# Kernel optimization log

Measured on AMD Instinct MI355X. Metric: run time of the kernel, lower is better.

## Reference

```python
import jax, jax.numpy as jnp
import numpy as np

B, S, HID = 2, 2048, 2048
NH = 16
Q_LORA, KV_LORA = 1024, 512
NOPE, ROPE, VD = 128, 64, 128
QK = NOPE + ROPE  # 192
EPS = 1e-6
THETA = 10000.0


def rms_norm(x, w, eps=EPS):
    x32 = x.astype(jnp.float32)
    var = jnp.mean(x32 * x32, axis=-1, keepdims=True)
    return (w * (x32 * jax.lax.rsqrt(var + eps))).astype(x.dtype)


def rotate_half(x):
    h = x.shape[-1] // 2
    return jnp.concatenate([-x[..., h:], x[..., :h]], axis=-1)


def setup_inputs() -> dict:
    key = jax.random.key(0)
    ks = jax.random.split(key, 8)
    hidden_states = jax.random.normal(ks[0], (B, S, HID), dtype=jnp.float32)
    attention_mask = jnp.zeros((B, 1, 1, S), dtype=jnp.float32)
    # RoPE tables (true rotary values)
    inv_freq = 1.0 / (THETA ** (np.arange(0, ROPE, 2, dtype=np.float32) / ROPE))
    pos = np.arange(S, dtype=np.float32)
    freqs = np.outer(pos, inv_freq)  # [S, ROPE/2]
    emb = np.concatenate([freqs, freqs], axis=-1)  # [S, ROPE]
    cos = jnp.asarray(np.cos(emb), dtype=jnp.float32)
    sin = jnp.asarray(np.sin(emb), dtype=jnp.float32)
    # Parameters, stored as [in, out] so y = x @ W
    sd = lambda fan_in: 1.0 / np.sqrt(fan_in)
    w_q_down = jax.random.normal(ks[1], (HID, Q_LORA), dtype=jnp.float32) * sd(HID)
    w_q_up = jax.random.normal(ks[2], (Q_LORA, NH * QK), dtype=jnp.float32) * sd(Q_LORA)
    w_kv_down = jax.random.normal(ks[3], (HID, KV_LORA + ROPE), dtype=jnp.float32) * sd(HID)
    w_kv_up = jax.random.normal(ks[4], (KV_LORA, NH * (NOPE + VD)), dtype=jnp.float32) * sd(KV_LORA)
    w_o = jax.random.normal(ks[5], (NH * VD, HID), dtype=jnp.float32) * sd(NH * VD)
    q_norm_w = jnp.ones((Q_LORA,), dtype=jnp.float32)
    kv_norm_w = jnp.ones((KV_LORA,), dtype=jnp.float32)
    return dict(hidden_states=hidden_states, attention_mask=attention_mask,
                cos=cos, sin=sin, w_q_down=w_q_down, w_q_up=w_q_up,
                w_kv_down=w_kv_down, w_kv_up=w_kv_up, w_o=w_o,
                q_norm_w=q_norm_w, kv_norm_w=kv_norm_w)


def reference(hidden_states, attention_mask, cos, sin,
              w_q_down, w_q_up, w_kv_down, w_kv_up, w_o,
              q_norm_w, kv_norm_w):
    b, s, _ = hidden_states.shape
    # --- Q path: down-proj -> RMSNorm -> up-proj ---
    q = rms_norm(hidden_states @ w_q_down, q_norm_w) @ w_q_up  # [b,s,NH*QK]
    q = q.reshape(b, s, NH, QK).transpose(0, 2, 1, 3)          # [b,h,s,QK]
    q_nope, q_rope = q[..., :NOPE], q[..., NOPE:]
    # --- KV path: down-proj -> split latent / rope key -> up-proj ---
    kv = hidden_states @ w_kv_down                              # [b,s,KV_LORA+ROPE]
    kv_latent, k_rope = kv[..., :KV_LORA], kv[..., KV_LORA:]
    kv_up = rms_norm(kv_latent, kv_norm_w) @ w_kv_up            # [b,s,NH*(NOPE+VD)]
    kv_up = kv_up.reshape(b, s, NH, NOPE + VD).transpose(0, 2, 1, 3)
    k_nope, v = kv_up[..., :NOPE], kv_up[..., NOPE:]            # [b,h,s,*]
    k_rope = k_rope[:, None, :, :]                              # [b,1,s,ROPE] (broadcast over heads)
    # --- partial RoPE ---
    c = cos[None, None, :, :]
    sn = sin[None, None, :, :]
    q_rope = q_rope * c + rotate_half(q_rope) * sn
    k_rope = k_rope * c + rotate_half(k_rope) * sn
    q_final = jnp.concatenate([q_nope, q_rope], axis=-1)        # [b,h,s,QK]
    k_final = jnp.concatenate([k_nope, jnp.broadcast_to(k_rope, (b, NH, s, ROPE))], axis=-1)
    # --- SDPA (non-causal, additive mask) ---
    scale = 1.0 / jnp.sqrt(jnp.asarray(QK, dtype=jnp.float32))
    scores = jnp.einsum('bhqd,bhkd->bhqk', q_final, k_final) * scale
    scores = scores + attention_mask                            # [b,1,1,s] broadcast
    probs = jax.nn.softmax(scores.astype(jnp.float32), axis=-1).astype(q_final.dtype)
    attn = jnp.einsum('bhqk,bhkd->bhqd', probs, v)              # [b,h,s,VD]
    attn = attn.transpose(0, 2, 1, 3).reshape(b, s, NH * VD)
    return attn @ w_o
```

## Files before the change

### kernel.cpp

```cpp
#include <hip/hip_runtime.h>
#include <hip/hip_bf16.h>

typedef unsigned short u16;
typedef unsigned int u32;
typedef short s16x8 __attribute__((ext_vector_type(8)));
typedef float f32x4 __attribute__((ext_vector_type(4)));
typedef float f32x2 __attribute__((ext_vector_type(2)));

__device__ __forceinline__ float bf2f(u16 u) {
    union { u32 i; float f; } v; v.i = ((u32)u) << 16; return v.f;
}
__device__ __forceinline__ u16 f2bf(float f) {
    union { float f; u32 i; } v; v.f = f;
    u32 i = v.i;
    u32 r = (i + 0x7FFFu + ((i >> 16) & 1u)) >> 16;
    return (u16)r;
}

__device__ __forceinline__ void gl2lds16(const u16* g, u16* l) {
    __builtin_amdgcn_global_load_lds(
        (const __attribute__((address_space(1))) u32*)g,
        (__attribute__((address_space(3))) u32*)l, 16, 0, 0);
}

__global__ __launch_bounds__(256) void cvt_f32_bf16(
    const float* __restrict__ in, u16* __restrict__ out, long long n2)
{
    long long i = (long long)blockIdx.x * 256 + threadIdx.x;
    if (i < n2) {
        f32x2 v = *(const f32x2*)(in + i * 2);
        u32 p = (u32)f2bf(v[0]) | ((u32)f2bf(v[1]) << 16);
        *(u32*)(out + i * 2) = p;
    }
}

__global__ __launch_bounds__(256) void transpose_f32_bf16(
    const float* __restrict__ in, u16* __restrict__ out, int R, int C)
{
    __shared__ u16 t[32][33];
    int tx = threadIdx.x & 31, ty = threadIdx.x >> 5;
    int c0 = blockIdx.x * 32, r0 = blockIdx.y * 32;
    #pragma unroll
    for (int i = 0; i < 32; i += 8)
        t[ty + i][tx] = f2bf(in[(size_t)(r0 + ty + i) * C + c0 + tx]);
    __syncthreads();
    #pragma unroll
    for (int i = 0; i < 32; i += 8)
        out[(size_t)(c0 + ty + i) * R + r0 + tx] = t[tx][ty + i];
}

__global__ __launch_bounds__(256) void transpose_v(
    const u16* __restrict__ kvup, u16* __restrict__ vt)
{
    __shared__ u16 t[32][33];
    int tx = threadIdx.x & 31, ty = threadIdx.x >> 5;
    int s0 = blockIdx.x * 32, v0 = blockIdx.y * 32;
    int b = blockIdx.z >> 4, h = blockIdx.z & 15;
    #pragma unroll
    for (int i = 0; i < 32; i += 8)
        t[ty + i][tx] = kvup[(size_t)(b * 2048 + s0 + ty + i) * 4096 + h * 256 + 128 + v0 + tx];
    __syncthreads();
    #pragma unroll
    for (int i = 0; i < 32; i += 8)
        vt[((size_t)(b * 16 + h) * 128 + v0 + ty + i) * 2048 + s0 + tx] = t[tx][ty + i];
}

__global__ __launch_bounds__(256) void gemm_bf16(
    const u16* __restrict__ A, const u16* __restrict__ Bt, u16* __restrict__ C,
    int M, int N, int K)
{
    __shared__ u16 As[64][40];
    __shared__ u16 Bs[64][40];

    const int tid  = threadIdx.x;
    const int wave = tid >> 6, lane = tid & 63;
    const int quad = lane >> 4, l16 = lane & 15;
    const int m0 = blockIdx.y * 64, n0 = blockIdx.x * 64;
    const int wm = (wave >> 1) * 32, wn = (wave & 1) * 32;

    const int srow = tid >> 2;
    const int koff = (tid & 3) * 8;

    f32x4 acc00 = {0.f,0.f,0.f,0.f};
    f32x4 acc01 = {0.f,0.f,0.f,0.f};
    f32x4 acc10 = {0.f,0.f,0.f,0.f};
    f32x4 acc11 = {0.f,0.f,0.f,0.f};

    for (int k0 = 0; k0 < K; k0 += 32) {
        *(s16x8*)&As[srow][koff] = *(const s16x8*)&A[(size_t)(m0 + srow) * K + k0 + koff];
        *(s16x8*)&Bs[srow][koff] = *(const s16x8*)&Bt[(size_t)(n0 + srow) * K + k0 + koff];
        __syncthreads();
        s16x8 a0 = *(const s16x8*)&As[wm + l16][quad * 8];
        s16x8 a1 = *(const s16x8*)&As[wm + 16 + l16][quad * 8];
        s16x8 b0 = *(const s16x8*)&Bs[wn + l16][quad * 8];
        s16x8 b1 = *(const s16x8*)&Bs[wn + 16 + l16][quad * 8];
        acc00 = __builtin_amdgcn_mfma_f32_16x16x32_bf16(a0, b0, acc00, 0, 0, 0);
        acc01 = __builtin_amdgcn_mfma_f32_16x16x32_bf16(a0, b1, acc01, 0, 0, 0);
        acc10 = __builtin_amdgcn_mfma_f32_16x16x32_bf16(a1, b0, acc10, 0, 0, 0);
        acc11 = __builtin_amdgcn_mfma_f32_16x16x32_bf16(a1, b1, acc11, 0, 0, 0);
        __syncthreads();
    }

    #pragma unroll
    for (int r = 0; r < 4; ++r) {
        int row0 = m0 + wm + quad * 4 + r;
        int col0 = n0 + wn + l16;
        C[(size_t)row0 * N + col0]             = f2bf(acc00[r]);
        C[(size_t)row0 * N + col0 + 16]        = f2bf(acc01[r]);
        C[(size_t)(row0 + 16) * N + col0]      = f2bf(acc10[r]);
        C[(size_t)(row0 + 16) * N + col0 + 16] = f2bf(acc11[r]);
    }
}

template <typename OUT>
__global__ __launch_bounds__(256) void gemm128(
    const u16* __restrict__ A, const u16* __restrict__ Bt, OUT* __restrict__ C,
    int M, int N, int K)
{
    __shared__ u16 As[128 * 32];
    __shared__ u16 Bs[128 * 32];

    const int tid  = threadIdx.x;
    const int wave = tid >> 6, lane = tid & 63;
    const int quad = lane >> 4, l16 = lane & 15;
    const int m0 = blockIdx.y * 128, n0 = blockIdx.x * 128;
    const int wm = (wave >> 1) * 64, wn = (wave & 1) * 64;

    const int srow = lane >> 2, soct = (lane & 3) * 8;

    f32x4 acc[4][4];
    #pragma unroll
    for (int i = 0; i < 4; ++i)
        #pragma unroll
        for (int j = 0; j < 4; ++j) acc[i][j] = (f32x4){0.f,0.f,0.f,0.f};

    for (int k0 = 0; k0 < K; k0 += 32) {
        #pragma unroll
        for (int op = 0; op < 2; ++op) {
            int g = wave * 2 + op;
            gl2lds16(&A[(size_t)(m0 + g * 16 + srow) * K + k0 + soct], &As[g * 512]);
            gl2lds16(&Bt[(size_t)(n0 + g * 16 + srow) * K + k0 + soct], &Bs[g * 512]);
        }
        __syncthreads();
        s16x8 af[4], bf[4];
        #pragma unroll
        for (int i = 0; i < 4; ++i) {
            af[i] = *(const s16x8*)&As[(wm + i * 16 + l16) * 32 + quad * 8];
            bf[i] = *(const s16x8*)&Bs[(wn + i * 16 + l16) * 32 + quad * 8];
        }
        #pragma unroll
        for (int i = 0; i < 4; ++i)
            #pragma unroll
            for (int j = 0; j < 4; ++j)
                acc[i][j] = __builtin_amdgcn_mfma_f32_16x16x32_bf16(af[i], bf[j], acc[i][j], 0, 0, 0);
        __syncthreads();
    }

    #pragma unroll
    for (int i = 0; i < 4; ++i) {
        #pragma unroll
        for (int j = 0; j < 4; ++j) {
            #pragma unroll
            for (int r = 0; r < 4; ++r) {
                int row = m0 + wm + i * 16 + quad * 4 + r;
                int col = n0 + wn + j * 16 + l16;
                if constexpr (sizeof(OUT) == 2)
                    C[(size_t)row * N + col] = f2bf(acc[i][j][r]);
                else
                    C[(size_t)row * N + col] = acc[i][j][r];
            }
        }
    }
}

__global__ __launch_bounds__(256) void rmsnorm_kernel(
    const u16* __restrict__ in, const float* __restrict__ w, u16* __restrict__ out,
    int len, int istride, int ostride)
{
    const int row = blockIdx.x, tid = threadIdx.x;
    const u16* x = in + (size_t)row * istride;
    float ss = 0.f;
    for (int i = tid; i < len; i += 256) { float v = bf2f(x[i]); ss += v * v; }
    #pragma unroll
    for (int off = 32; off >= 1; off >>= 1) ss += __shfl_xor(ss, off, 64);
    __shared__ float wsum[4];
    if ((tid & 63) == 0) wsum[tid >> 6] = ss;
    __syncthreads();
    float tot = wsum[0] + wsum[1] + wsum[2] + wsum[3];
    float inv = 1.0f / sqrtf(tot / (float)len + 1e-6f);
    for (int i = tid; i < len; i += 256) {
        float v = bf2f(x[i]);
        out[(size_t)row * ostride + i] = f2bf(v * inv * w[i]);
    }
}

__global__ __launch_bounds__(256) void rope_kernel(
    u16* __restrict__ qb, const u16* __restrict__ kvb, u16* __restrict__ krot,
    const float* __restrict__ cosb, const float* __restrict__ sinb)
{
    const int row = blockIdx.x;
    const int s = row & 2047;
    const int lane = threadIdx.x & 63, wave = threadIdx.x >> 6;
    const float c  = cosb[s * 64 + lane];
    const float sn = sinb[s * 64 + lane];
    for (int seg = wave; seg < 17; seg += 4) {
        const u16* pin; u16* pout;
        if (seg < 16) { pout = qb + (size_t)row * 3072 + seg * 192 + 128; pin = pout; }
        else          { pin = kvb + (size_t)row * 576 + 512; pout = krot + (size_t)row * 64; }
        float x  = bf2f(pin[lane]);
        float xp = bf2f(pin[lane ^ 32]);
        float rot = (lane < 32) ? -xp : xp;
        pout[lane] = f2bf(x * c + rot * sn);
    }
}

__global__ __launch_bounds__(256) void attn_mfma2(
    const u16* __restrict__ qb,
    const u16* __restrict__ kvup,
    const u16* __restrict__ krot,
    const u16* __restrict__ vt,
    const float* __restrict__ mask,
    u16* __restrict__ attnb)
{
    __shared__ u16 Ks[64][200];
    __shared__ u16 Vs[128][72];
    __shared__ u16 Ps[64][72];

    const int tid  = threadIdx.x;
    const int wave = tid >> 6, lane = tid & 63;
    const int quad = lane >> 4, l16 = lane & 15;
    const int qt = blockIdx.x, h = blockIdx.y, b = blockIdx.z;
    const int row0 = b * 2048 + qt * 64;
    const int qw = wave * 16;
    const float scale = 0.07216878364870323f;

    s16x8 qf[6];
    #pragma unroll
    for (int kc = 0; kc < 6; ++kc)
        qf[kc] = *(const s16x8*)&qb[(size_t)(row0 + qw + l16) * 3072 + h * 192 + kc * 32 + quad * 8];

    float m[4], l[4];
    #pragma unroll
    for (int r = 0; r < 4; ++r) { m[r] = -__builtin_inff(); l[r] = 0.f; }
    f32x4 O[8];
    #pragma unroll
    for (int vi = 0; vi < 8; ++vi) O[vi] = (f32x4){0.f,0.f,0.f,0.f};

    const u16* vtb = vt + ((size_t)(b * 16 + h) * 128) * 2048;

    for (int kt = 0; kt < 32; ++kt) {
        const int krow0 = b * 2048 + kt * 64;
        __syncthreads();
        #pragma unroll
        for (int i = 0; i < 6; ++i) {
            int idx = tid + i * 256;
            int r = idx / 24, c = (idx % 24) * 8;
            const u16* src = (c < 128)
                ? &kvup[(size_t)(krow0 + r) * 4096 + h * 256 + c]
                : &krot[(size_t)(krow0 + r) * 64 + (c - 128)];
            *(s16x8*)&Ks[r][c] = *(const s16x8*)src;
        }
        #pragma unroll
        for (int i = 0; i < 4; ++i) {
            int idx = tid + i * 256;
            int r = idx >> 3, c8 = (idx & 7) * 8;
            *(s16x8*)&Vs[r][c8] = *(const s16x8*)&vtb[(size_t)r * 2048 + kt * 64 + c8];
        }
        __syncthreads();

        f32x4 S[4];
        #pragma unroll
        for (int ct = 0; ct < 4; ++ct) S[ct] = (f32x4){0.f,0.f,0.f,0.f};
        #pragma unroll
        for (int kc = 0; kc < 6; ++kc) {
            #pragma unroll
            for (int ct = 0; ct < 4; ++ct) {
                s16x8 bf = *(const s16x8*)&Ks[ct * 16 + l16][kc * 32 + quad * 8];
                S[ct] = __builtin_amdgcn_mfma_f32_16x16x32_bf16(qf[kc], bf, S[ct], 0, 0, 0);
            }
        }
        #pragma unroll
        for (int ct = 0; ct < 4; ++ct) {
            float mv = mask[b * 2048 + kt * 64 + ct * 16 + l16];
            #pragma unroll
            for (int r = 0; r < 4; ++r) S[ct][r] = S[ct][r] * scale + mv;
        }
        float tmax[4];
        #pragma unroll
        for (int r = 0; r < 4; ++r)
            tmax[r] = fmaxf(fmaxf(S[0][r], S[1][r]), fmaxf(S[2][r], S[3][r]));
        #pragma unroll
        for (int off = 1; off < 16; off <<= 1) {
            #pragma unroll
            for (int r = 0; r < 4; ++r)
                tmax[r] = fmaxf(tmax[r], __shfl_xor(tmax[r], off, 64));
        }
        float alpha[4];
        #pragma unroll
        for (int r = 0; r < 4; ++r) {
            float mn = fmaxf(m[r], tmax[r]);
            alpha[r] = __expf(m[r] - mn);
            m[r] = mn;
        }
        float rsum[4] = {0.f, 0.f, 0.f, 0.f};
        #pragma unroll
        for (int ct = 0; ct < 4; ++ct) {
            #pragma unroll
            for (int r = 0; r < 4; ++r) {
                float p = __expf(S[ct][r] - m[r]);
                S[ct][r] = p;
                rsum[r] += p;
            }
        }
        #pragma unroll
        for (int off = 1; off < 16; off <<= 1) {
            #pragma unroll
            for (int r = 0; r < 4; ++r)
                rsum[r] += __shfl_xor(rsum[r], off, 64);
        }
        #pragma unroll
        for (int r = 0; r < 4; ++r) l[r] = l[r] * alpha[r] + rsum[r];
        #pragma unroll
        for (int ct = 0; ct < 4; ++ct) {
            #pragma unroll
            for (int r = 0; r < 4; ++r)
                Ps[qw + quad * 4 + r][ct * 16 + l16] = f2bf(S[ct][r]);
        }
        #pragma unroll
        for (int vi = 0; vi < 8; ++vi) {
            #pragma unroll
            for (int r = 0; r < 4; ++r) O[vi][r] *= alpha[r];
        }
        #pragma unroll
        for (int kc = 0; kc < 2; ++kc) {
            s16x8 a = *(const s16x8*)&Ps[qw + l16][kc * 32 + quad * 8];
            #pragma unroll
            for (int vi = 0; vi < 8; ++vi) {
                s16x8 bf = *(const s16x8*)&Vs[vi * 16 + l16][kc * 32 + quad * 8];
                O[vi] = __builtin_amdgcn_mfma_f32_16x16x32_bf16(a, bf, O[vi], 0, 0, 0);
            }
        }
    }

    float linv[4];
    #pragma unroll
    for (int r = 0; r < 4; ++r) linv[r] = 1.0f / l[r];
    #pragma unroll
    for (int vi = 0; vi < 8; ++vi) {
        #pragma unroll
        for (int r = 0; r < 4; ++r) {
            int q_ = row0 + qw + quad * 4 + r;
            attnb[(size_t)q_ * 2048 + h * 128 + vi * 16 + l16] = f2bf(O[vi][r] * linv[r]);
        }
    }
}

extern "C" void kernel_launch(void* const* d_in, const int* in_sizes, int n_in,
                              void* d_out, int out_size, void* d_ws, size_t ws_size,
                              hipStream_t stream)
{
    const float* hidden = (const float*)d_in[0];
    const float* mask   = (const float*)d_in[1];
    const float* cosb   = (const float*)d_in[2];
    const float* sinb   = (const float*)d_in[3];
    const float* w_qd   = (const float*)d_in[4];
    const float* w_qu   = (const float*)d_in[5];
    const float* w_kvd  = (const float*)d_in[6];
    const float* w_kvu  = (const float*)d_in[7];
    const float* w_o    = (const float*)d_in[8];
    const float* qnw    = (const float*)d_in[9];
    const float* kvnw   = (const float*)d_in[10];
    float* out = (float*)d_out;

    u16* ws = (u16*)d_ws;
    u16* qbuf   = ws + 0;
    u16* wt_qd  = ws + 0;
    u16* kvup   = ws + 12582912;
    u16* hid_bf = ws + 12582912;
    u16* wt_kvd = ws + 20971520;
    u16* attnb  = ws + 29360128;
    u16* qd     = ws + 29360128;
    u16* wt_qu  = ws + 33554432;
    u16* kvb    = ws + 37748736;
    u16* wt_o   = ws + 37748736;
    u16* kvn    = ws + 40108032;
    u16* wt_kvu = ws + 42205184;
    u16* krot   = ws + 44302336;
    u16* vt     = ws + 44564480;

    {
        long long n2 = (long long)4096 * 2048 / 2;
        cvt_f32_bf16<<<(int)((n2 + 255) / 256), 256, 0, stream>>>(hidden, hid_bf, n2);
    }

    transpose_f32_bf16<<<dim3(32, 64), 256, 0, stream>>>(w_qd, wt_qd, 2048, 1024);
    gemm128<u16><<<dim3(8, 32), 256, 0, stream>>>(hid_bf, wt_qd, qd, 4096, 1024, 2048);
    rmsnorm_kernel<<<4096, 256, 0, stream>>>(qd, qnw, qd, 1024, 1024, 1024);
    transpose_f32_bf16<<<dim3(96, 32), 256, 0, stream>>>(w_qu, wt_qu, 1024, 3072);
    gemm128<u16><<<dim3(24, 32), 256, 0, stream>>>(qd, wt_qu, qbuf, 4096, 3072, 1024);

    transpose_f32_bf16<<<dim3(18, 64), 256, 0, stream>>>(w_kvd, wt_kvd, 2048, 576);
    gemm_bf16<<<dim3(9, 64), 256, 0, stream>>>(hid_bf, wt_kvd, kvb, 4096, 576, 2048);
    rmsnorm_kernel<<<4096, 256, 0, stream>>>(kvb, kvnw, kvn, 512, 576, 512);
    transpose_f32_bf16<<<dim3(128, 16), 256, 0, stream>>>(w_kvu, wt_kvu, 512, 4096);
    gemm128<u16><<<dim3(32, 32), 256, 0, stream>>>(kvn, wt_kvu, kvup, 4096, 4096, 512);

    transpose_v<<<dim3(64, 4, 32), 256, 0, stream>>>(kvup, vt);

    rope_kernel<<<4096, 256, 0, stream>>>(qbuf, kvb, krot, cosb, sinb);
    transpose_f32_bf16<<<dim3(64, 64), 256, 0, stream>>>(w_o, wt_o, 2048, 2048);

    attn_mfma2<<<dim3(32, 16, 2), 256, 0, stream>>>(qbuf, kvup, krot, vt, mask, attnb);

    gemm128<float><<<dim3(16, 32), 256, 0, stream>>>(attnb, wt_o, out, 4096, 2048, 2048);
}
```

Baseline: 598.2 us.

## Process 128 query rows per attention block with a shared softmax max

Result: faster. 520.3 us (-13.0%).

```diff
diff --git a/kernel.cpp b/kernel.cpp
--- a/kernel.cpp
+++ b/kernel.cpp
@@ -214,7 +214,7 @@
     }
 }
 
-__global__ __launch_bounds__(256) void attn_mfma2(
+__global__ __launch_bounds__(256, 2) void attn_mfma3(
     const u16* __restrict__ qb,
     const u16* __restrict__ kvup,
     const u16* __restrict__ krot,
@@ -224,27 +224,35 @@
 {
     __shared__ u16 Ks[64][200];
     __shared__ u16 Vs[128][72];
-    __shared__ u16 Ps[64][72];
+    __shared__ u16 Ps[128][72];
 
     const int tid  = threadIdx.x;
     const int wave = tid >> 6, lane = tid & 63;
     const int quad = lane >> 4, l16 = lane & 15;
     const int qt = blockIdx.x, h = blockIdx.y, b = blockIdx.z;
-    const int row0 = b * 2048 + qt * 64;
+    const int row0 = b * 2048 + qt * 128;
     const int qw = wave * 16;
     const float scale = 0.07216878364870323f;
 
-    s16x8 qf[6];
-    #pragma unroll
-    for (int kc = 0; kc < 6; ++kc)
-        qf[kc] = *(const s16x8*)&qb[(size_t)(row0 + qw + l16) * 3072 + h * 192 + kc * 32 + quad * 8];
-
-    float m[4], l[4];
-    #pragma unroll
-    for (int r = 0; r < 4; ++r) { m[r] = -__builtin_inff(); l[r] = 0.f; }
-    f32x4 O[8];
-    #pragma unroll
-    for (int vi = 0; vi < 8; ++vi) O[vi] = (f32x4){0.f,0.f,0.f,0.f};
+    s16x8 onesf;
+    #pragma unroll
+    for (int j = 0; j < 8; ++j) onesf[j] = (short)0x3F80;
+
+    s16x8 qf[2][6];
+    #pragma unroll
+    for (int s = 0; s < 2; ++s)
+        #pragma unroll
+        for (int kc = 0; kc < 6; ++kc)
+            qf[s][kc] = *(const s16x8*)&qb[(size_t)(row0 + s * 64 + qw + l16) * 3072
+                                           + h * 192 + kc * 32 + quad * 8];
+
+    float m = -__builtin_inff();
+    f32x4 l[2] = {(f32x4){0.f,0.f,0.f,0.f}, (f32x4){0.f,0.f,0.f,0.f}};
+    f32x4 O[2][8];
+    #pragma unroll
+    for (int s = 0; s < 2; ++s)
+        #pragma unroll
+        for (int vi = 0; vi < 8; ++vi) O[s][vi] = (f32x4){0.f,0.f,0.f,0.f};
 
     const u16* vtb = vt + ((size_t)(b * 16 + h) * 128) * 2048;
 
@@ -268,89 +276,81 @@
         }
         __syncthreads();
 
-        f32x4 S[4];
-        #pragma unroll
-        for (int ct = 0; ct < 4; ++ct) S[ct] = (f32x4){0.f,0.f,0.f,0.f};
+        f32x4 S[2][4];
+        #pragma unroll
+        for (int s = 0; s < 2; ++s)
+            #pragma unroll
+            for (int ct = 0; ct < 4; ++ct) S[s][ct] = (f32x4){0.f,0.f,0.f,0.f};
         #pragma unroll
         for (int kc = 0; kc < 6; ++kc) {
             #pragma unroll
             for (int ct = 0; ct < 4; ++ct) {
                 s16x8 bf = *(const s16x8*)&Ks[ct * 16 + l16][kc * 32 + quad * 8];
-                S[ct] = __builtin_amdgcn_mfma_f32_16x16x32_bf16(qf[kc], bf, S[ct], 0, 0, 0);
+                S[0][ct] = __builtin_amdgcn_mfma_f32_16x16x32_bf16(qf[0][kc], bf, S[0][ct], 0, 0, 0);
+                S[1][ct] = __builtin_amdgcn_mfma_f32_16x16x32_bf16(qf[1][kc], bf, S[1][ct], 0, 0, 0);
             }
         }
         #pragma unroll
         for (int ct = 0; ct < 4; ++ct) {
             float mv = mask[b * 2048 + kt * 64 + ct * 16 + l16];
             #pragma unroll
-            for (int r = 0; r < 4; ++r) S[ct][r] = S[ct][r] * scale + mv;
-        }
-        float tmax[4];
-        #pragma unroll
-        for (int r = 0; r < 4; ++r)
-            tmax[r] = fmaxf(fmaxf(S[0][r], S[1][r]), fmaxf(S[2][r], S[3][r]));
-        #pragma unroll
-        for (int off = 1; off < 16; off <<= 1) {
-            #pragma unroll
-            for (int r = 0; r < 4; ++r)
-                tmax[r] = fmaxf(tmax[r], __shfl_xor(tmax[r], off, 64));
-        }
-        float alpha[4];
-        #pragma unroll
-        for (int r = 0; r < 4; ++r) {
-            float mn = fmaxf(m[r], tmax[r]);
-            alpha[r] = __expf(m[r] - mn);
-            m[r] = mn;
-        }
-        float rsum[4] = {0.f, 0.f, 0.f, 0.f};
-        #pragma unroll
-        for (int ct = 0; ct < 4; ++ct) {
-            #pragma unroll
-            for (int r = 0; r < 4; ++r) {
-                float p = __expf(S[ct][r] - m[r]);
-                S[ct][r] = p;
-                rsum[r] += p;
-            }
-        }
-        #pragma unroll
-        for (int off = 1; off < 16; off <<= 1) {
-            #pragma unroll
-            for (int r = 0; r < 4; ++r)
-                rsum[r] += __shfl_xor(rsum[r], off, 64);
-        }
-        #pragma unroll
-        for (int r = 0; r < 4; ++r) l[r] = l[r] * alpha[r] + rsum[r];
-        #pragma unroll
-        for (int ct = 0; ct < 4; ++ct) {
-            #pragma unroll
-            for (int r = 0; r < 4; ++r)
-                Ps[qw + quad * 4 + r][ct * 16 + l16] = f2bf(S[ct][r]);
-        }
-        #pragma unroll
-        for (int vi = 0; vi < 8; ++vi) {
-            #pragma unroll
-            for (int r = 0; r < 4; ++r) O[vi][r] *= alpha[r];
+            for (int s = 0; s < 2; ++s)
+                #pragma unroll
+                for (int r = 0; r < 4; ++r) S[s][ct][r] = S[s][ct][r] * scale + mv;
+        }
+        float tm = S[0][0][0];
+        #pragma unroll
+        for (int s = 0; s < 2; ++s)
+            #pragma unroll
+            for (int ct = 0; ct < 4; ++ct)
+                #pragma unroll
+                for (int r = 0; r < 4; ++r) tm = fmaxf(tm, S[s][ct][r]);
+        #pragma unroll
+        for (int off = 1; off < 64; off <<= 1)
+            tm = fmaxf(tm, __shfl_xor(tm, off, 64));
+        float mn = fmaxf(m, tm);
+        float alpha = __expf(m - mn);
+        m = mn;
+        #pragma unroll
+        for (int s = 0; s < 2; ++s)
+            #pragma unroll
+            for (int ct = 0; ct < 4; ++ct)
+                #pragma unroll
+                for (int r = 0; r < 4; ++r)
+                    Ps[s * 64 + qw + quad * 4 + r][ct * 16 + l16] = f2bf(__expf(S[s][ct][r] - m));
+        #pragma unroll
+        for (int s = 0; s < 2; ++s) {
+            l[s] *= alpha;
+            #pragma unroll
+            for (int vi = 0; vi < 8; ++vi) O[s][vi] *= alpha;
         }
         #pragma unroll
         for (int kc = 0; kc < 2; ++kc) {
-            s16x8 a = *(const s16x8*)&Ps[qw + l16][kc * 32 + quad * 8];
+            s16x8 a0 = *(const s16x8*)&Ps[qw + l16][kc * 32 + quad * 8];
+            s16x8 a1 = *(const s16x8*)&Ps[64 + qw + l16][kc * 32 + quad * 8];
             #pragma unroll
             for (int vi = 0; vi < 8; ++vi) {
                 s16x8 bf = *(const s16x8*)&Vs[vi * 16 + l16][kc * 32 + quad * 8];
-                O[vi] = __builtin_amdgcn_mfma_f32_16x16x32_bf16(a, bf, O[vi], 0, 0, 0);
+                O[0][vi] = __builtin_amdgcn_mfma_f32_16x16x32_bf16(a0, bf, O[0][vi], 0, 0, 0);
+                O[1][vi] = __builtin_amdgcn_mfma_f32_16x16x32_bf16(a1, bf, O[1][vi], 0, 0, 0);
             }
-        }
-    }
-
-    float linv[4];
-    #pragma unroll
-    for (int r = 0; r < 4; ++r) linv[r] = 1.0f / l[r];
-    #pragma unroll
-    for (int vi = 0; vi < 8; ++vi) {
-        #pragma unroll
-        for (int r = 0; r < 4; ++r) {
-            int q_ = row0 + qw + quad * 4 + r;
-            attnb[(size_t)q_ * 2048 + h * 128 + vi * 16 + l16] = f2bf(O[vi][r] * linv[r]);
+            l[0] = __builtin_amdgcn_mfma_f32_16x16x32_bf16(a0, onesf, l[0], 0, 0, 0);
+            l[1] = __builtin_amdgcn_mfma_f32_16x16x32_bf16(a1, onesf, l[1], 0, 0, 0);
+        }
+    }
+
+    #pragma unroll
+    for (int s = 0; s < 2; ++s) {
+        f32x4 linv;
+        #pragma unroll
+        for (int r = 0; r < 4; ++r) linv[r] = 1.0f / l[s][r];
+        #pragma unroll
+        for (int vi = 0; vi < 8; ++vi) {
+            #pragma unroll
+            for (int r = 0; r < 4; ++r) {
+                int q_ = row0 + s * 64 + qw + quad * 4 + r;
+                attnb[(size_t)q_ * 2048 + h * 128 + vi * 16 + l16] = f2bf(O[s][vi][r] * linv[r]);
+            }
         }
     }
 }
@@ -410,7 +410,7 @@
     rope_kernel<<<4096, 256, 0, stream>>>(qbuf, kvb, krot, cosb, sinb);
     transpose_f32_bf16<<<dim3(64, 64), 256, 0, stream>>>(w_o, wt_o, 2048, 2048);
 
-    attn_mfma2<<<dim3(32, 16, 2), 256, 0, stream>>>(qbuf, kvup, krot, vt, mask, attnb);
+    attn_mfma3<<<dim3(16, 16, 2), 256, 0, stream>>>(qbuf, kvup, krot, vt, mask, attnb);
 
     gemm128<float><<<dim3(16, 32), 256, 0, stream>>>(attnb, wt_o, out, 4096, 2048, 2048);
 }
```
